# Performance work log

Hardware: AMD Instinct MI355X
Metric: run time of the kernel (lower is better)

## Reference

```python
import jax, jax.numpy as jnp
import numpy as np

HIDDEN = 1024
HEADS = 16
HEAD_DIM = HIDDEN // HEADS
SEQ = 2048
BATCH = 2


def setup_inputs() -> dict:
    key = jax.random.key(0)
    ks = jax.random.split(key, 11)
    s = 1.0 / np.sqrt(HIDDEN)
    inp = {
        'query': jax.random.normal(ks[0], (SEQ, BATCH, HIDDEN), jnp.float32),
        'key': jax.random.normal(ks[1], (SEQ, BATCH, HIDDEN), jnp.float32),
        'value': jax.random.normal(ks[2], (SEQ, BATCH, HIDDEN), jnp.float32),
        'Wq': jax.random.normal(ks[3], (HIDDEN, HIDDEN), jnp.float32) * s,
        'bq': jnp.zeros((HIDDEN,), jnp.float32),
        'Wk': jax.random.normal(ks[4], (HIDDEN, HIDDEN), jnp.float32) * s,
        'bk': jnp.zeros((HIDDEN,), jnp.float32),
        'Wv': jax.random.normal(ks[5], (HIDDEN, HIDDEN), jnp.float32) * s,
        'bv': jnp.zeros((HIDDEN,), jnp.float32),
        'Wo': jax.random.normal(ks[6], (HIDDEN, HIDDEN), jnp.float32) * s,
        'bo': jnp.zeros((HIDDEN,), jnp.float32),
    }
    return inp


def reference(query, key, value, Wq, bq, Wk, bk, Wv, bv, Wo, bo):
    # Linear layers: torch Linear computes x @ W.T + b
    S, B, _ = query.shape
    q = (query @ Wq.T + bq).reshape(S, B, HEADS, HEAD_DIM)
    k = (key @ Wk.T + bk).reshape(S, B, HEADS, HEAD_DIM)
    v = (value @ Wv.T + bv).reshape(S, B, HEADS, HEAD_DIM)
    # -> [B, H, S, D]
    q = jnp.transpose(q, (1, 2, 0, 3))
    k = jnp.transpose(k, (1, 2, 0, 3))
    v = jnp.transpose(v, (1, 2, 0, 3))
    scores = jnp.einsum('bhqd,bhkd->bhqk', q, k) / np.sqrt(HEAD_DIM)
    attn = jax.nn.softmax(scores, axis=-1)  # dropout=0.0 -> identity
    out = jnp.einsum('bhqk,bhkd->bhqd', attn, v)
    out = jnp.transpose(out, (2, 0, 1, 3)).reshape(S, B, HIDDEN)
    out = out @ Wo.T + bo
    return out, attn
```

## Files before the change

### kernel.cpp

```cpp
#include <hip/hip_runtime.h>
#include <hip/hip_bf16.h>
#include <cstdint>
#include <cstddef>

#define SEQLEN 2048
#define NBATCH 2
#define NHEAD  16
#define HDIM   64
#define HID    1024
#define MROWS  4096

typedef __bf16 bf16x8 __attribute__((ext_vector_type(8)));
typedef float f32x4 __attribute__((ext_vector_type(4)));
typedef unsigned short ushort8 __attribute__((ext_vector_type(8)));

#define MFMA16(a, b, c) __builtin_amdgcn_mfma_f32_16x16x32_bf16((a), (b), (c), 0, 0, 0)

#define GLOAD_LDS16(g, l)                                                        \
    __builtin_amdgcn_global_load_lds(                                            \
        (const __attribute__((address_space(1))) void*)(g),                      \
        (__attribute__((address_space(3))) void*)(l), 16, 0, 0)

#define SBAR() __builtin_amdgcn_s_barrier()
#define SCHED_FENCE() __builtin_amdgcn_sched_barrier(0)
#define WAIT_VMCNT(n) asm volatile("s_waitcnt vmcnt(" #n ")" ::: "memory")

static __device__ __forceinline__ unsigned int pack_bf16_pair(float lo, float hi) {
    unsigned short a = __builtin_bit_cast(unsigned short, (__bf16)lo);
    unsigned short b = __builtin_bit_cast(unsigned short, (__bf16)hi);
    return ((unsigned int)b << 16) | a;
}

__global__ __launch_bounds__(256) void conv6(
    const float* __restrict__ s0, const float* __restrict__ s1, const float* __restrict__ s2,
    const float* __restrict__ s3, const float* __restrict__ s4, const float* __restrict__ s5,
    unsigned short* __restrict__ Sc)
{
    const int y = blockIdx.y;
    const float* src = (y == 0) ? s0 : (y == 1) ? s1 : (y == 2) ? s2
                     : (y == 3) ? s3 : (y == 4) ? s4 : s5;
    const size_t M1 = 1u << 20;
    unsigned short* dst = (y < 3) ? (Sc + (size_t)y * 4 * M1) : (Sc + 12 * M1 + (size_t)(y - 3) * M1);
    const size_t n = (y < 3) ? 4 * M1 : M1;

    const size_t i = ((size_t)blockIdx.x * 256 + threadIdx.x) * 8;
    if (i >= n) return;
    float4 f0 = *(const float4*)(src + i);
    float4 f1 = *(const float4*)(src + i + 4);
    ushort8 o;
    o[0] = __builtin_bit_cast(unsigned short, (__bf16)f0.x);
    o[1] = __builtin_bit_cast(unsigned short, (__bf16)f0.y);
    o[2] = __builtin_bit_cast(unsigned short, (__bf16)f0.z);
    o[3] = __builtin_bit_cast(unsigned short, (__bf16)f0.w);
    o[4] = __builtin_bit_cast(unsigned short, (__bf16)f1.x);
    o[5] = __builtin_bit_cast(unsigned short, (__bf16)f1.y);
    o[6] = __builtin_bit_cast(unsigned short, (__bf16)f1.z);
    o[7] = __builtin_bit_cast(unsigned short, (__bf16)f1.w);
    *(ushort8*)(dst + i) = o;
}

__global__ __launch_bounds__(256) void wconv(
    const float* __restrict__ Wo, unsigned short* __restrict__ Wob)
{
    const size_t i = ((size_t)blockIdx.x * 256 + threadIdx.x) * 8;
    float4 f0 = *(const float4*)(Wo + i);
    float4 f1 = *(const float4*)(Wo + i + 4);
    ushort8 o;
    o[0] = __builtin_bit_cast(unsigned short, (__bf16)f0.x);
    o[1] = __builtin_bit_cast(unsigned short, (__bf16)f0.y);
    o[2] = __builtin_bit_cast(unsigned short, (__bf16)f0.z);
    o[3] = __builtin_bit_cast(unsigned short, (__bf16)f0.w);
    o[4] = __builtin_bit_cast(unsigned short, (__bf16)f1.x);
    o[5] = __builtin_bit_cast(unsigned short, (__bf16)f1.y);
    o[6] = __builtin_bit_cast(unsigned short, (__bf16)f1.z);
    o[7] = __builtin_bit_cast(unsigned short, (__bf16)f1.w);
    *(ushort8*)(Wob + i) = o;
}

#define GSTAGE32(DSTARR, SRCP, k0v)                                              \
    _Pragma("unroll")                                                            \
    for (int c_ = 0; c_ < 2; ++c_) {                                             \
        const int row_ = (c_ << 6) + (threadIdx.x >> 2);                         \
        const unsigned short* gs_ = (SRCP) + (size_t)row_ * HID + (k0v)          \
            + ((((int)threadIdx.x & 3) ^ ((row_ >> 1) & 3)) << 3);               \
        GLOAD_LDS16(gs_, &(DSTARR)[((c_ << 6) + (((int)threadIdx.x >> 6) << 4)) * 32]); \
    }

#define GEMM_BODY(ApT, BpT)                                                      \
    GSTAGE32(As[0], ApT, 0);                                                     \
    GSTAGE32(Bs[0], BpT, 0);                                                     \
    for (int it = 0; it < 32; ++it) {                                            \
        SBAR();                                                                  \
        const int k1 = ((it + 1) & 31) << 5;                                     \
        GSTAGE32(As[(it + 1) & 1], ApT, k1);                                     \
        GSTAGE32(Bs[(it + 1) & 1], BpT, k1);                                     \
        WAIT_VMCNT(8);                                                           \
        SBAR();                                                                  \
        SCHED_FENCE();                                                           \
        const char* Ac = (const char*)As[it & 1];                                \
        const char* Bc = (const char*)Bs[it & 1];                                \
        bf16x8 a_h[4], b_h[4];                                                   \
        _Pragma("unroll")                                                        \
        for (int m = 0; m < 4; ++m) {                                            \
            const int row = wm * 64 + m * 16 + fr;                               \
            a_h[m] = *(const bf16x8*)(Ac + (row << 6) + ((fg ^ ((row >> 1) & 3)) << 4)); \
        }                                                                        \
        _Pragma("unroll")                                                        \
        for (int n = 0; n < 4; ++n) {                                            \
            const int row = wn * 64 + n * 16 + fr;                               \
            b_h[n] = *(const bf16x8*)(Bc + (row << 6) + ((fg ^ ((row >> 1) & 3)) << 4)); \
        }                                                                        \
        __builtin_amdgcn_s_setprio(1);                                           \
        _Pragma("unroll")                                                        \
        for (int m = 0; m < 4; ++m)                                              \
            _Pragma("unroll")                                                    \
            for (int n = 0; n < 4; ++n)                                          \
                acc[m][n] = MFMA16(a_h[m], b_h[n], acc[m][n]);                   \
        __builtin_amdgcn_s_setprio(0);                                           \
    }

__global__ __launch_bounds__(256) void qkv_gemm(
    const unsigned short* __restrict__ Sc,
    const float* __restrict__ bq, const float* __restrict__ bk, const float* __restrict__ bv,
    unsigned short* __restrict__ Qb, unsigned short* __restrict__ Kb, unsigned short* __restrict__ Vb)
{
    const int z = blockIdx.z;
    const size_t M1 = 1u << 20;
    const unsigned short* A = Sc + (size_t)z * 4 * M1;
    const unsigned short* B = Sc + 12 * M1 + (size_t)z * M1;
    const float* bias = (z == 0) ? bq : (z == 1) ? bk : bv;
    unsigned short* dst = (z == 0) ? Qb : (z == 1) ? Kb : Vb;

    __shared__ unsigned short As[2][128 * 32];
    __shared__ unsigned short Bs[2][128 * 32];

    const int t = threadIdx.x, lane = t & 63, w = t >> 6;
    const int wm = w >> 1, wn = w & 1;
    const int bm = blockIdx.x * 128, bn = blockIdx.y * 128;
    const int fr = lane & 15, fg = lane >> 4;

    const unsigned short* Ap = A + (size_t)bm * HID;
    const unsigned short* Bp = B + (size_t)bn * HID;

    f32x4 acc[4][4] = {};
    GEMM_BODY(Ap, Bp)

    #pragma unroll
    for (int n = 0; n < 4; ++n) {
        const int gc = bn + wn * 64 + n * 16 + fr;
        const float bb = bias[gc];
        #pragma unroll
        for (int m = 0; m < 4; ++m)
            #pragma unroll
            for (int r = 0; r < 4; ++r) {
                const int gr = bm + wm * 64 + m * 16 + fg * 4 + r;
                *(__bf16*)&dst[(size_t)gr * HID + gc] = (__bf16)(acc[m][n][r] + bb);
            }
    }
}

__global__ __launch_bounds__(256) void vtrans(
    const unsigned short* __restrict__ Vb, unsigned short* __restrict__ Vt)
{
    __shared__ unsigned short T[64][66];
    const int t = threadIdx.x;
    const int s0 = blockIdx.x * 64, h = blockIdx.y, b = blockIdx.z;

    {
        const int s_l = t >> 2, d0 = (t & 3) * 16;
        const unsigned short* src = Vb + (((size_t)(s0 + s_l) * 2 + b) << 10) + (h << 6) + d0;
        *(ushort8*)&T[s_l][d0]     = *(const ushort8*)src;
        *(ushort8*)&T[s_l][d0 + 8] = *(const ushort8*)(src + 8);
    }
    __syncthreads();
    {
        const int d_l = t >> 2, sc = (t & 3) * 16;
        ushort8 o0, o1;
        #pragma unroll
        for (int j = 0; j < 8; ++j) { o0[j] = T[sc + j][d_l]; o1[j] = T[sc + 8 + j][d_l]; }
        unsigned short* dst = Vt + (((size_t)((b << 4) + h) * 64 + d_l) << 11) + s0 + sc;
        *(ushort8*)dst       = o0;
        *(ushort8*)(dst + 8) = o1;
    }
}

#define STAGE_K1(ktv)                                                            \
    {                                                                            \
        const int kti_ = (ktv);                                                  \
        _Pragma("unroll")                                                        \
        for (int c_ = 0; c_ < 4; ++c_) {                                         \
            const int rb_ = (w << 5) + (c_ << 3);                                \
            const int rl_ = rb_ + (lane >> 3);                                   \
            const unsigned short* ks_ = Kb + (((size_t)((kti_ << 7) + rl_) * 2 + b) << 10) \
                + (h << 6) + (((lane & 7) ^ (rl_ & 7)) << 3);                    \
            GLOAD_LDS16(ks_, &Ks[rb_ * 64]);                                     \
        }                                                                        \
    }

__global__ __launch_bounds__(256) void attn2(
    const unsigned short* __restrict__ Qb, const unsigned short* __restrict__ Kb,
    const unsigned short* __restrict__ Vt, float* __restrict__ attn_out,
    unsigned short* __restrict__ Hb)
{
    __shared__ unsigned short Ks[128 * 64];
    __shared__ unsigned short Pl[4][16 * 128];

    const int flat = blockIdx.x + (blockIdx.y << 5) + (blockIdx.z << 9);
    const int nf = (flat & 7) * 128 + (flat >> 3);
    const int qblk = nf & 31, h = (nf >> 5) & 15, b = nf >> 9;

    const int t = threadIdx.x, lane = t & 63, w = t >> 6;
    const int fr = lane & 15, fg = lane >> 4;
    const int fg4 = fg << 2, fg16 = fg << 4;
    const int qbase = qblk * 64 + w * 16;
    const float c_exp = 0.18033688011112042f;

    bf16x8 qf[2];
    {
        const int q = qbase + fr;
        const unsigned short* qp = Qb + (((size_t)q * 2 + b) << 10) + (h << 6);
        qf[0] = *(const bf16x8*)(qp + (fg << 3));
        qf[1] = *(const bf16x8*)(qp + 32 + (fg << 3));
    }

    char* Plc = (char*)&Pl[w][0];
    float lsum = 0.f;

    for (int kt = 0; kt < 16; ++kt) {
        __syncthreads();
        STAGE_K1(kt);
        __syncthreads();

        const char* Kc = (const char*)Ks;
        f32x4 s_[8] = {};
        __builtin_amdgcn_s_setprio(1);
        #pragma unroll
        for (int n = 0; n < 8; ++n) {
            const int row = (n << 4) + fr;
            const int rx = (row & 7) << 4;
            #pragma unroll
            for (int kk = 0; kk < 2; ++kk) {
                bf16x8 kf = *(const bf16x8*)(Kc + (row << 7) + (((kk << 6) | fg16) ^ rx));
                s_[n] = MFMA16(kf, qf[kk], s_[n]);
            }
        }
        __builtin_amdgcn_s_setprio(0);

        float a = 0.f;
        #pragma unroll
        for (int n = 0; n < 8; ++n)
            #pragma unroll
            for (int r = 0; r < 4; ++r)
                a += exp2f(s_[n][r] * c_exp);
        lsum += a;
    }

    float li;
    {
        float v = lsum;
        v += __shfl_xor(v, 16);
        v += __shfl_xor(v, 32);
        li = -__log2f(v);
    }

    f32x4 oacc[4] = {};
    float* attnB = attn_out + ((size_t)((b << 4) + h) << 22);
    const size_t vhead = (size_t)((b << 4) + h) << 6;
    const int rxl = (fr & 7) << 4;

    for (int kt = 0; kt < 16; ++kt) {
        __syncthreads();
        STAGE_K1(kt);
        __syncthreads();

        const char* Kc = (const char*)Ks;
        f32x4 s_[8] = {};
        __builtin_amdgcn_s_setprio(1);
        #pragma unroll
        for (int n = 0; n < 8; ++n) {
            const int row = (n << 4) + fr;
            const int rx = (row & 7) << 4;
            #pragma unroll
            for (int kk = 0; kk < 2; ++kk) {
                bf16x8 kf = *(const bf16x8*)(Kc + (row << 7) + (((kk << 6) | fg16) ^ rx));
                s_[n] = MFMA16(kf, qf[kk], s_[n]);
            }
        }
        __builtin_amdgcn_s_setprio(0);

        float* ab = attnB + ((size_t)(qbase + fr) << 11) + (kt << 7) + fg4;
        #pragma unroll
        for (int n = 0; n < 8; ++n) {
            f32x4 p;
            #pragma unroll
            for (int r = 0; r < 4; ++r)
                p[r] = exp2f(__builtin_fmaf(s_[n][r], c_exp, li));
            *(f32x4*)(ab + (n << 4)) = p;
            uint2 pk;
            pk.x = pack_bf16_pair(p[0], p[1]);
            pk.y = pack_bf16_pair(p[2], p[3]);
            *(uint2*)(Plc + (fr << 8) + (((n << 5) | (fg << 3)) ^ rxl)) = pk;
        }

        __builtin_amdgcn_s_setprio(1);
        #pragma unroll
        for (int kk2 = 0; kk2 < 4; ++kk2) {
            bf16x8 pa = *(const bf16x8*)(Plc + (fr << 8) + (((kk2 << 6) | fg16) ^ rxl));
            #pragma unroll
            for (int n2 = 0; n2 < 4; ++n2) {
                bf16x8 vf = *(const bf16x8*)(Vt + ((vhead + (n2 << 4) + fr) << 11)
                                             + (kt << 7) + (kk2 << 5) + (fg << 3));
                oacc[n2] = MFMA16(pa, vf, oacc[n2]);
            }
        }
        __builtin_amdgcn_s_setprio(0);
    }

    #pragma unroll
    for (int n2 = 0; n2 < 4; ++n2)
        #pragma unroll
        for (int r = 0; r < 4; ++r) {
            const int q = qbase + fg4 + r;
            *(__bf16*)&Hb[(((size_t)q * 2 + b) << 10) + (h << 6) + (n2 << 4) + fr] =
                (__bf16)oacc[n2][r];
        }
}

__global__ __launch_bounds__(256) void out_proj(
    const unsigned short* __restrict__ Hb, const unsigned short* __restrict__ Wob,
    const float* __restrict__ bo, float* __restrict__ out)
{
    __shared__ unsigned short As[2][128 * 32];
    __shared__ unsigned short Bs[2][128 * 32];

    const int t = threadIdx.x, lane = t & 63, w = t >> 6;
    const int wm = w >> 1, wn = w & 1;
    const int bm = blockIdx.x * 128, bn = blockIdx.y * 128;
    const int fr = lane & 15, fg = lane >> 4;

    const unsigned short* Ap = Hb + (size_t)bm * HID;
    const unsigned short* Bp = Wob + (size_t)bn * HID;

    f32x4 acc[4][4] = {};
    GEMM_BODY(Ap, Bp)

    #pragma unroll
    for (int n = 0; n < 4; ++n) {
        const int gc = bn + wn * 64 + n * 16 + fr;
        const float bb = bo[gc];
        #pragma unroll
        for (int m = 0; m < 4; ++m)
            #pragma unroll
            for (int r = 0; r < 4; ++r) {
                const int gr = bm + wm * 64 + m * 16 + fg * 4 + r;
                out[(size_t)gr * HID + gc] = acc[m][n][r] + bb;
            }
    }
}

extern "C" void kernel_launch(void* const* d_in, const int* in_sizes, int n_in,
                              void* d_out, int out_size, void* d_ws, size_t ws_size,
                              hipStream_t stream)
{
    (void)in_sizes; (void)n_in; (void)out_size;

    const float* query = (const float*)d_in[0];
    const float* key   = (const float*)d_in[1];
    const float* value = (const float*)d_in[2];
    const float* bq    = (const float*)d_in[4];
    const float* bk    = (const float*)d_in[6];
    const float* bv    = (const float*)d_in[8];
    const float* Wo    = (const float*)d_in[9];
    const float* bo    = (const float*)d_in[10];

    float* out0 = (float*)d_out;
    float* attn = out0 + (size_t)MROWS * HID;

    if (ws_size < (size_t)32 * 1024 * 1024) return;
    const size_t nbuf = (size_t)MROWS * HID;
    unsigned short* Qb = (unsigned short*)d_ws;
    unsigned short* Kb = Qb + nbuf;
    unsigned short* Vb = Kb + nbuf;
    unsigned short* Vt = Vb + nbuf;
    unsigned short* Hb = Vb;
    unsigned short* Wob = Qb;

    unsigned short* Sc = (unsigned short*)attn;

    conv6<<<dim3(2048, 6), 256, 0, stream>>>(query, key, value,
                                             (const float*)d_in[3], (const float*)d_in[5],
                                             (const float*)d_in[7], Sc);
    qkv_gemm<<<dim3(32, 8, 3), 256, 0, stream>>>(Sc, bq, bk, bv, Qb, Kb, Vb);
    vtrans<<<dim3(32, NHEAD, NBATCH), 256, 0, stream>>>(Vb, Vt);
    attn2<<<dim3(32, NHEAD, NBATCH), 256, 0, stream>>>(Qb, Kb, Vt, attn, Hb);
    wconv<<<dim3(512), 256, 0, stream>>>(Wo, Wob);
    out_proj<<<dim3(32, 8), 256, 0, stream>>>(Hb, Wob, bo, out0);
}
```

Before: 338.8 us.

## Load K fragments directly from global memory instead of staging through LDS

Drops the shared-memory K tile, its async global-to-LDS staging and the two block barriers per tile in both attention passes. Each wave now reads its K fragments straight from global memory (relying on L2/L1 for reuse across the four waves), and the s_setprio hints are removed. This removes barrier stalls and LDS traffic but raises global/cache load traffic fourfold for K, with uncoalesced per-lane 16-byte loads strided by row.

```diff
diff --git a/kernel.cpp b/kernel.cpp
--- a/kernel.cpp
+++ b/kernel.cpp
@@ -184,25 +184,11 @@
     }
 }
 
-#define STAGE_K1(ktv)                                                            \
-    {                                                                            \
-        const int kti_ = (ktv);                                                  \
-        _Pragma("unroll")                                                        \
-        for (int c_ = 0; c_ < 4; ++c_) {                                         \
-            const int rb_ = (w << 5) + (c_ << 3);                                \
-            const int rl_ = rb_ + (lane >> 3);                                   \
-            const unsigned short* ks_ = Kb + (((size_t)((kti_ << 7) + rl_) * 2 + b) << 10) \
-                + (h << 6) + (((lane & 7) ^ (rl_ & 7)) << 3);                    \
-            GLOAD_LDS16(ks_, &Ks[rb_ * 64]);                                     \
-        }                                                                        \
-    }
-
 __global__ __launch_bounds__(256) void attn2(
     const unsigned short* __restrict__ Qb, const unsigned short* __restrict__ Kb,
     const unsigned short* __restrict__ Vt, float* __restrict__ attn_out,
     unsigned short* __restrict__ Hb)
 {
-    __shared__ unsigned short Ks[128 * 64];
     __shared__ unsigned short Pl[4][16 * 128];
 
     const int flat = blockIdx.x + (blockIdx.y << 5) + (blockIdx.z << 9);
@@ -217,35 +203,26 @@
 
     bf16x8 qf[2];
     {
-        const int q = qbase + fr;
-        const unsigned short* qp = Qb + (((size_t)q * 2 + b) << 10) + (h << 6);
+        const unsigned short* qp = Qb + (((size_t)(qbase + fr) * 2 + b) << 10) + (h << 6);
         qf[0] = *(const bf16x8*)(qp + (fg << 3));
         qf[1] = *(const bf16x8*)(qp + 32 + (fg << 3));
     }
 
+    const unsigned short* kbase = Kb + (((size_t)fr * 2 + b) << 10) + (h << 6) + (fg << 3);
+
     char* Plc = (char*)&Pl[w][0];
     float lsum = 0.f;
 
     for (int kt = 0; kt < 16; ++kt) {
-        __syncthreads();
-        STAGE_K1(kt);
-        __syncthreads();
-
-        const char* Kc = (const char*)Ks;
         f32x4 s_[8] = {};
-        __builtin_amdgcn_s_setprio(1);
         #pragma unroll
         for (int n = 0; n < 8; ++n) {
-            const int row = (n << 4) + fr;
-            const int rx = (row & 7) << 4;
-            #pragma unroll
-            for (int kk = 0; kk < 2; ++kk) {
-                bf16x8 kf = *(const bf16x8*)(Kc + (row << 7) + (((kk << 6) | fg16) ^ rx));
-                s_[n] = MFMA16(kf, qf[kk], s_[n]);
-            }
-        }
-        __builtin_amdgcn_s_setprio(0);
-
+            const unsigned short* kr = kbase + ((size_t)((kt << 7) + (n << 4)) << 11);
+            bf16x8 k0 = *(const bf16x8*)kr;
+            bf16x8 k1 = *(const bf16x8*)(kr + 32);
+            s_[n] = MFMA16(k0, qf[0], s_[n]);
+            s_[n] = MFMA16(k1, qf[1], s_[n]);
+        }
         float a = 0.f;
         #pragma unroll
         for (int n = 0; n < 8; ++n)
@@ -269,24 +246,15 @@
     const int rxl = (fr & 7) << 4;
 
     for (int kt = 0; kt < 16; ++kt) {
-        __syncthreads();
-        STAGE_K1(kt);
-        __syncthreads();
-
-        const char* Kc = (const char*)Ks;
         f32x4 s_[8] = {};
-        __builtin_amdgcn_s_setprio(1);
         #pragma unroll
         for (int n = 0; n < 8; ++n) {
-            const int row = (n << 4) + fr;
-            const int rx = (row & 7) << 4;
-            #pragma unroll
-            for (int kk = 0; kk < 2; ++kk) {
-                bf16x8 kf = *(const bf16x8*)(Kc + (row << 7) + (((kk << 6) | fg16) ^ rx));
-                s_[n] = MFMA16(kf, qf[kk], s_[n]);
-            }
-        }
-        __builtin_amdgcn_s_setprio(0);
+            const unsigned short* kr = kbase + ((size_t)((kt << 7) + (n << 4)) << 11);
+            bf16x8 k0 = *(const bf16x8*)kr;
+            bf16x8 k1 = *(const bf16x8*)(kr + 32);
+            s_[n] = MFMA16(k0, qf[0], s_[n]);
+            s_[n] = MFMA16(k1, qf[1], s_[n]);
+        }
 
         float* ab = attnB + ((size_t)(qbase + fr) << 11) + (kt << 7) + fg4;
         #pragma unroll
@@ -302,7 +270,6 @@
             *(uint2*)(Plc + (fr << 8) + (((n << 5) | (fg << 3)) ^ rxl)) = pk;
         }
 
-        __builtin_amdgcn_s_setprio(1);
         #pragma unroll
         for (int kk2 = 0; kk2 < 4; ++kk2) {
             bf16x8 pa = *(const bf16x8*)(Plc + (fr << 8) + (((kk2 << 6) | fg16) ^ rxl));
@@ -313,7 +280,6 @@
                 oacc[n2] = MFMA16(pa, vf, oacc[n2]);
             }
         }
-        __builtin_amdgcn_s_setprio(0);
     }
 
     #pragma unroll
```

Result: slower. 496.7 us (+46.6%).

## Split attention into single-pass PV kernel and separate probability-store kernel

Applied to the files above, without the earlier changes.

The two-pass attention kernel is split in two. The first kernel computes unnormalized exp scores, accumulates the row sum and the PV product in one pass, then normalizes the output at the end and stashes the log row sum in the attn buffer. A second kernel recomputes QK^T with larger 256-row K tiles and writes the normalized probabilities. This decouples the PV work from the large fp32 attn store, at the cost of an extra launch, recomputed QK, and a scratch value kept in the attn output. Skipping the max subtraction relies on scores staying small enough that the exponentials do not overflow.

```diff
diff --git a/kernel.cpp b/kernel.cpp
--- a/kernel.cpp
+++ b/kernel.cpp
@@ -197,7 +197,7 @@
         }                                                                        \
     }
 
-__global__ __launch_bounds__(256) void attn2(
+__global__ __launch_bounds__(256) void attn_pv(
     const unsigned short* __restrict__ Qb, const unsigned short* __restrict__ Kb,
     const unsigned short* __restrict__ Vt, float* __restrict__ attn_out,
     unsigned short* __restrict__ Hb)
@@ -217,14 +217,17 @@
 
     bf16x8 qf[2];
     {
-        const int q = qbase + fr;
-        const unsigned short* qp = Qb + (((size_t)q * 2 + b) << 10) + (h << 6);
+        const unsigned short* qp = Qb + (((size_t)(qbase + fr) * 2 + b) << 10) + (h << 6);
         qf[0] = *(const bf16x8*)(qp + (fg << 3));
         qf[1] = *(const bf16x8*)(qp + 32 + (fg << 3));
     }
 
     char* Plc = (char*)&Pl[w][0];
+    const size_t vhead = (size_t)((b << 4) + h) << 6;
+    const int rxl = (fr & 7) << 4;
+
     float lsum = 0.f;
+    f32x4 oacc[4] = {};
 
     for (int kt = 0; kt < 16; ++kt) {
         __syncthreads();
@@ -248,59 +251,18 @@
 
         float a = 0.f;
         #pragma unroll
-        for (int n = 0; n < 8; ++n)
-            #pragma unroll
-            for (int r = 0; r < 4; ++r)
-                a += exp2f(s_[n][r] * c_exp);
-        lsum += a;
-    }
-
-    float li;
-    {
-        float v = lsum;
-        v += __shfl_xor(v, 16);
-        v += __shfl_xor(v, 32);
-        li = -__log2f(v);
-    }
-
-    f32x4 oacc[4] = {};
-    float* attnB = attn_out + ((size_t)((b << 4) + h) << 22);
-    const size_t vhead = (size_t)((b << 4) + h) << 6;
-    const int rxl = (fr & 7) << 4;
-
-    for (int kt = 0; kt < 16; ++kt) {
-        __syncthreads();
-        STAGE_K1(kt);
-        __syncthreads();
-
-        const char* Kc = (const char*)Ks;
-        f32x4 s_[8] = {};
-        __builtin_amdgcn_s_setprio(1);
-        #pragma unroll
-        for (int n = 0; n < 8; ++n) {
-            const int row = (n << 4) + fr;
-            const int rx = (row & 7) << 4;
-            #pragma unroll
-            for (int kk = 0; kk < 2; ++kk) {
-                bf16x8 kf = *(const bf16x8*)(Kc + (row << 7) + (((kk << 6) | fg16) ^ rx));
-                s_[n] = MFMA16(kf, qf[kk], s_[n]);
-            }
-        }
-        __builtin_amdgcn_s_setprio(0);
-
-        float* ab = attnB + ((size_t)(qbase + fr) << 11) + (kt << 7) + fg4;
-        #pragma unroll
         for (int n = 0; n < 8; ++n) {
             f32x4 p;
             #pragma unroll
             for (int r = 0; r < 4; ++r)
-                p[r] = exp2f(__builtin_fmaf(s_[n][r], c_exp, li));
-            *(f32x4*)(ab + (n << 4)) = p;
+                p[r] = exp2f(s_[n][r] * c_exp);
+            a += (p[0] + p[1]) + (p[2] + p[3]);
             uint2 pk;
             pk.x = pack_bf16_pair(p[0], p[1]);
             pk.y = pack_bf16_pair(p[2], p[3]);
             *(uint2*)(Plc + (fr << 8) + (((n << 5) | (fg << 3)) ^ rxl)) = pk;
         }
+        lsum += a;
 
         __builtin_amdgcn_s_setprio(1);
         #pragma unroll
@@ -316,14 +278,96 @@
         __builtin_amdgcn_s_setprio(0);
     }
 
+    float v = lsum;
+    v += __shfl_xor(v, 16);
+    v += __shfl_xor(v, 32);
+    const float inv = 1.f / v;
+    const float li = -__log2f(v);
+
+    float* attnB = attn_out + ((size_t)((b << 4) + h) << 22);
+    if (fg == 0)
+        attnB[(size_t)(qbase + fr) << 11] = li;
+
+    float iq[4];
+    #pragma unroll
+    for (int r = 0; r < 4; ++r) iq[r] = __shfl(inv, fg4 + r);
+
     #pragma unroll
     for (int n2 = 0; n2 < 4; ++n2)
         #pragma unroll
         for (int r = 0; r < 4; ++r) {
             const int q = qbase + fg4 + r;
             *(__bf16*)&Hb[(((size_t)q * 2 + b) << 10) + (h << 6) + (n2 << 4) + fr] =
-                (__bf16)oacc[n2][r];
-        }
+                (__bf16)(oacc[n2][r] * iq[r]);
+        }
+}
+
+__global__ __launch_bounds__(256) void attn_store(
+    const unsigned short* __restrict__ Qb, const unsigned short* __restrict__ Kb,
+    float* __restrict__ attn_out)
+{
+    __shared__ unsigned short Ks[256 * 64];
+
+    const int flat = blockIdx.x + (blockIdx.y << 5) + (blockIdx.z << 9);
+    const int nf = (flat & 7) * 128 + (flat >> 3);
+    const int qblk = nf & 31, h = (nf >> 5) & 15, b = nf >> 9;
+
+    const int t = threadIdx.x, lane = t & 63, w = t >> 6;
+    const int fr = lane & 15, fg = lane >> 4;
+    const int fg4 = fg << 2, fg16 = fg << 4;
+    const int qbase = qblk * 64 + w * 16;
+    const float c_exp = 0.18033688011112042f;
+
+    bf16x8 qf[2];
+    {
+        const unsigned short* qp = Qb + (((size_t)(qbase + fr) * 2 + b) << 10) + (h << 6);
+        qf[0] = *(const bf16x8*)(qp + (fg << 3));
+        qf[1] = *(const bf16x8*)(qp + 32 + (fg << 3));
+    }
+
+    float* attnB = attn_out + ((size_t)((b << 4) + h) << 22);
+    const float li = attnB[(size_t)(qbase + fr) << 11];
+
+    for (int kt2 = 0; kt2 < 8; ++kt2) {
+        __syncthreads();
+        #pragma unroll
+        for (int c_ = 0; c_ < 8; ++c_) {
+            const int rb_ = (w << 6) + (c_ << 3);
+            const int rl_ = rb_ + (lane >> 3);
+            const unsigned short* ks_ = Kb + (((size_t)((kt2 << 8) + rl_) * 2 + b) << 10)
+                + (h << 6) + (((lane & 7) ^ (rl_ & 7)) << 3);
+            GLOAD_LDS16(ks_, &Ks[rb_ * 64]);
+        }
+        __syncthreads();
+
+        const char* Kc = (const char*)Ks;
+        #pragma unroll
+        for (int half = 0; half < 2; ++half) {
+            f32x4 s_[8] = {};
+            __builtin_amdgcn_s_setprio(1);
+            #pragma unroll
+            for (int n = 0; n < 8; ++n) {
+                const int row = (half << 7) + (n << 4) + fr;
+                const int rx = (row & 7) << 4;
+                #pragma unroll
+                for (int kk = 0; kk < 2; ++kk) {
+                    bf16x8 kf = *(const bf16x8*)(Kc + (row << 7) + (((kk << 6) | fg16) ^ rx));
+                    s_[n] = MFMA16(kf, qf[kk], s_[n]);
+                }
+            }
+            __builtin_amdgcn_s_setprio(0);
+
+            float* ab = attnB + ((size_t)(qbase + fr) << 11) + (kt2 << 8) + (half << 7) + fg4;
+            #pragma unroll
+            for (int n = 0; n < 8; ++n) {
+                f32x4 p;
+                #pragma unroll
+                for (int r = 0; r < 4; ++r)
+                    p[r] = exp2f(__builtin_fmaf(s_[n][r], c_exp, li));
+                *(f32x4*)(ab + (n << 4)) = p;
+            }
+        }
+    }
 }
 
 __global__ __launch_bounds__(256) void out_proj(
@@ -392,7 +436,8 @@
                                              (const float*)d_in[7], Sc);
     qkv_gemm<<<dim3(32, 8, 3), 256, 0, stream>>>(Sc, bq, bk, bv, Qb, Kb, Vb);
     vtrans<<<dim3(32, NHEAD, NBATCH), 256, 0, stream>>>(Vb, Vt);
-    attn2<<<dim3(32, NHEAD, NBATCH), 256, 0, stream>>>(Qb, Kb, Vt, attn, Hb);
+    attn_pv<<<dim3(32, NHEAD, NBATCH), 256, 0, stream>>>(Qb, Kb, Vt, attn, Hb);
+    attn_store<<<dim3(32, NHEAD, NBATCH), 256, 0, stream>>>(Qb, Kb, attn);
     wconv<<<dim3(512), 256, 0, stream>>>(Wo, Wob);
     out_proj<<<dim3(32, 8), 256, 0, stream>>>(Hb, Wob, bo, out0);
 }
```

Result: slower. 356.7 us (+5.3%).
